# Optimization experiments

Measured on AMD Instinct MI355X. Metric: run time of the kernel, lower is better.

The kernel has to match this reference:

```python
import jax, jax.numpy as jnp
import numpy as np

G = 256          # voxel grid resolution per axis (single batch item)
N = 400000       # number of active voxels
C_IN, C_OUT = 32, 64
EPS = 1e-5


def _build_neighbor_maps():
    """Emulates torchsparse's hash-based kernel map for a 3x3x3, stride-1 conv.
    Returns int32 [27, N]: nbr_idx[k, i] = input voxel index at coords[i]+offset_k, or -1."""
    rng = np.random.default_rng(0)
    lin = rng.choice(G ** 3, size=N, replace=False).astype(np.int64)  # unique active voxels
    coords = np.stack(np.unravel_index(lin, (G, G, G)), axis=1)       # [N,3]
    order = np.argsort(lin)
    keys_sorted = lin[order]
    # 27 kernel offsets in {-1,0,1}^3
    offs = np.stack(np.meshgrid(*[np.arange(-1, 2)] * 3, indexing='ij'), axis=-1).reshape(27, 3)
    q = coords[None, :, :] + offs[:, None, :]                          # [27,N,3]
    inb = np.all((q >= 0) & (q < G), axis=-1)                          # [27,N]
    qc = np.clip(q, 0, G - 1)
    nk = (qc[..., 0] * G + qc[..., 1]) * G + qc[..., 2]                # [27,N]
    pos = np.searchsorted(keys_sorted, nk.ravel()).reshape(27, N)
    posc = np.minimum(pos, N - 1)
    found = inb & (keys_sorted[posc] == nk)
    nbr = np.where(found, order[posc], -1).astype(np.int32)
    return nbr


def setup_inputs() -> dict:
    key = jax.random.key(0)
    k1, k2 = jax.random.split(key)
    features = jax.random.normal(k1, (N, C_IN), dtype=jnp.float32)
    gamma = jnp.ones((C_IN,), jnp.float32)
    beta = jnp.zeros((C_IN,), jnp.float32)
    W = jax.random.normal(k2, (27, C_IN, C_OUT), dtype=jnp.float32) * 0.05
    nbr_idx = jnp.asarray(_build_neighbor_maps())
    return {"features": features, "gamma": gamma, "beta": beta, "W": W, "nbr_idx": nbr_idx}


def reference(features, gamma, beta, W, nbr_idx):
    # BatchNorm1d (training-mode batch stats) over active voxels
    mean = jnp.mean(features, axis=0)
    var = jnp.var(features, axis=0)
    x = gamma * (features - mean) * jax.lax.rsqrt(var + EPS) + beta
    x = jax.nn.relu(x)
    # Sparse 3x3x3 conv: per-offset gather -> GEMM -> accumulate (scatter is identity
    # since stride=1 keeps output coords == input coords).
    out0 = jnp.zeros((x.shape[0], W.shape[-1]), dtype=x.dtype)

    def body(acc, kw):
        idx, Wk = kw                                  # idx: [N], Wk: [C_in, C_out]
        valid = (idx >= 0)[:, None]
        g = jnp.where(valid, x[jnp.maximum(idx, 0)], 0.0)  # gather with masking
        return acc + g @ Wk, None

    out, _ = jax.lax.scan(body, out0, (nbr_idx, W))
    return out
```

## Files before the change

kernel.cpp:

```cpp
#include <hip/hip_runtime.h>
#include <hip/hip_bf16.h>

#define CIN  32
#define COUT 64
#define KVOL 27
#define FEPS 1e-5f

typedef __attribute__((ext_vector_type(8))) short short8;
typedef __attribute__((ext_vector_type(4))) float f32x4;


__device__ __forceinline__ unsigned bfr(float f) {
    unsigned u = __float_as_uint(f);
    return (u + 0x7FFFu + ((u >> 16) & 1u)) >> 16;
}

__global__ void k_zero(float* __restrict__ ws) {
    if (threadIdx.x < 64) ws[threadIdx.x] = 0.f;
}

__global__ __launch_bounds__(256) void k_reduce(const float* __restrict__ f,
                                                float* __restrict__ ws, int n4) {
    const float4* f4 = (const float4*)f;
    int tid    = blockIdx.x * blockDim.x + threadIdx.x;
    int stride = gridDim.x * blockDim.x;
    float4 s = make_float4(0.f, 0.f, 0.f, 0.f);
    float4 q = make_float4(0.f, 0.f, 0.f, 0.f);
    for (int i = tid; i < n4; i += stride) {
        float4 v = f4[i];
        s.x += v.x; s.y += v.y; s.z += v.z; s.w += v.w;
        q.x = fmaf(v.x, v.x, q.x); q.y = fmaf(v.y, v.y, q.y);
        q.z = fmaf(v.z, v.z, q.z); q.w = fmaf(v.w, v.w, q.w);
    }
    __shared__ float ls[64];
    if (threadIdx.x < 64) ls[threadIdx.x] = 0.f;
    __syncthreads();
    int g = threadIdx.x & 7;
    atomicAdd(&ls[g * 4 + 0], s.x); atomicAdd(&ls[g * 4 + 1], s.y);
    atomicAdd(&ls[g * 4 + 2], s.z); atomicAdd(&ls[g * 4 + 3], s.w);
    atomicAdd(&ls[32 + g * 4 + 0], q.x); atomicAdd(&ls[32 + g * 4 + 1], q.y);
    atomicAdd(&ls[32 + g * 4 + 2], q.z); atomicAdd(&ls[32 + g * 4 + 3], q.w);
    __syncthreads();
    if (threadIdx.x < 64) atomicAdd(&ws[threadIdx.x], ls[threadIdx.x]);
}

__global__ void k_final(const float* __restrict__ gamma, const float* __restrict__ beta,
                        float* __restrict__ ws, float invN) {
    int c = threadIdx.x;
    float mean = ws[c] * invN;
    float var  = fmaf(-mean, mean, ws[32 + c] * invN);
    float sc   = gamma[c] * rsqrtf(var + FEPS);
    ws[64 + c] = sc;
    ws[96 + c] = fmaf(-mean, sc, beta[c]);
}

__global__ __launch_bounds__(256) void k_norm(const float* __restrict__ f,
                                              const float* __restrict__ ws,
                                              uint4* __restrict__ xb, int n8) {
    const float4* f4 = (const float4*)f;
    int tid    = blockIdx.x * blockDim.x + threadIdx.x;
    int stride = gridDim.x * blockDim.x;
    int g = tid & 3;
    float4 s0 = ((const float4*)(ws + 64))[2 * g];
    float4 s1 = ((const float4*)(ws + 64))[2 * g + 1];
    float4 b0 = ((const float4*)(ws + 96))[2 * g];
    float4 b1 = ((const float4*)(ws + 96))[2 * g + 1];
    for (int i = tid; i < n8; i += stride) {
        float4 v0 = f4[2 * i], v1 = f4[2 * i + 1];
        v0.x = fmaxf(fmaf(v0.x, s0.x, b0.x), 0.f);
        v0.y = fmaxf(fmaf(v0.y, s0.y, b0.y), 0.f);
        v0.z = fmaxf(fmaf(v0.z, s0.z, b0.z), 0.f);
        v0.w = fmaxf(fmaf(v0.w, s0.w, b0.w), 0.f);
        v1.x = fmaxf(fmaf(v1.x, s1.x, b1.x), 0.f);
        v1.y = fmaxf(fmaf(v1.y, s1.y, b1.y), 0.f);
        v1.z = fmaxf(fmaf(v1.z, s1.z, b1.z), 0.f);
        v1.w = fmaxf(fmaf(v1.w, s1.w, b1.w), 0.f);
        uint4 r;
        r.x = bfr(v0.x) | (bfr(v0.y) << 16);
        r.y = bfr(v0.z) | (bfr(v0.w) << 16);
        r.z = bfr(v1.x) | (bfr(v1.y) << 16);
        r.w = bfr(v1.z) | (bfr(v1.w) << 16);
        xb[i] = r;
    }
}

__global__ __launch_bounds__(256) void k_prep(const float* __restrict__ W,
                                              uint4* __restrict__ Bf) {
    int k    = blockIdx.x;
    int nt   = threadIdx.x >> 6;
    int lane = threadIdx.x & 63;
    int col  = nt * 16 + (lane & 15);
    int kk   = (lane >> 4) * 8;
    const float* Wk = W + (size_t)k * (CIN * COUT);
    unsigned r[4];
#pragma unroll
    for (int e = 0; e < 4; ++e) {
        unsigned lo = bfr(Wk[(kk + 2 * e) * COUT + col]);
        unsigned hi = bfr(Wk[(kk + 2 * e + 1) * COUT + col]);
        r[e] = lo | (hi << 16);
    }
    Bf[(size_t)(k * 4 + nt) * 64 + lane] = make_uint4(r[0], r[1], r[2], r[3]);
}

#define GROUP_A(X) X(0,A) X(1,B) X(2,A) X(3,B) X(4,A) X(5,B) X(6,A) X(7,B) X(8,A)
#define GROUP_B(X) X(9,B) X(10,A) X(11,B) X(12,A) X(13,B) X(14,A) X(15,B) X(16,A) X(17,B)
#define GROUP_C(X) X(18,A) X(19,B) X(20,A) X(21,B) X(22,A) X(23,B) X(24,A) X(25,B) X(26,A)

#define KDECL(K,P) int idx##K; uint4 ga##K;
#define KIDX(K,P)  idx##K = nbrl[(size_t)(K) * n];
#define KGATH(K,P) ga##K = *(const uint4*)(xhb + ((size_t)((idx##K < 0) ? 0 : idx##K) << 6) + koff);
#define KPIN(K,P)  asm volatile("" : "+v"(ga##K.x), "+v"(ga##K.y), "+v"(ga##K.z), "+v"(ga##K.w));
#define KCONS(K,P) { uint4 z##K = (idx##K < 0) ? zero4 : ga##K;                                 \
    if (__ballot(idx##K >= 0)) {                                                                \
        short8 av = __builtin_bit_cast(short8, z##K);                                           \
        short8 b0 = __builtin_bit_cast(short8, Bs[(K) * 256 + lane]);                           \
        short8 b1 = __builtin_bit_cast(short8, Bs[(K) * 256 + 64 + lane]);                      \
        short8 b2 = __builtin_bit_cast(short8, Bs[(K) * 256 + 128 + lane]);                     \
        short8 b3 = __builtin_bit_cast(short8, Bs[(K) * 256 + 192 + lane]);                     \
        acc0##P = __builtin_amdgcn_mfma_f32_16x16x32_bf16(av, b0, acc0##P, 0, 0, 0);            \
        acc1##P = __builtin_amdgcn_mfma_f32_16x16x32_bf16(av, b1, acc1##P, 0, 0, 0);            \
        acc2##P = __builtin_amdgcn_mfma_f32_16x16x32_bf16(av, b2, acc2##P, 0, 0, 0);            \
        acc3##P = __builtin_amdgcn_mfma_f32_16x16x32_bf16(av, b3, acc3##P, 0, 0, 0);            \
    } }

__global__ __launch_bounds__(512, 2) void k_conv(const char* __restrict__ xhb,
                                                 const uint4* __restrict__ Bf,
                                                 const int* __restrict__ nbr,
                                                 float* __restrict__ out,
                                                 int n, int ntiles) {
    __shared__ uint4 Bs[KVOL * 256];
    int lane = threadIdx.x & 63;
    int wv   = threadIdx.x >> 6;

    for (int t = threadIdx.x; t < KVOL * 256; t += 512) Bs[t] = Bf[t];
    __syncthreads();

    int gw   = blockIdx.x * 8 + wv;
    int col  = lane & 15;
    int koff = (lane >> 4) * 16;
    const uint4 zero4 = make_uint4(0u, 0u, 0u, 0u);

    for (int t = gw; t < ntiles; t += 2048) {
        int r0 = t * 16;
        const int* nbrl = nbr + (r0 + col);

        f32x4 zf = {0.f, 0.f, 0.f, 0.f};
        f32x4 acc0A = zf, acc1A = zf, acc2A = zf, acc3A = zf;
        f32x4 acc0B = zf, acc1B = zf, acc2B = zf, acc3B = zf;

        GROUP_A(KDECL) GROUP_B(KDECL) GROUP_C(KDECL)
        GROUP_A(KIDX)  GROUP_B(KIDX)  GROUP_C(KIDX)
        GROUP_A(KGATH) GROUP_B(KGATH) GROUP_C(KGATH)
        GROUP_A(KPIN)
        GROUP_A(KCONS)
        GROUP_B(KPIN)
        GROUP_B(KCONS)
        GROUP_C(KPIN)
        GROUP_C(KCONS)

        f32x4 acc0 = acc0A + acc0B;
        f32x4 acc1 = acc1A + acc1B;
        f32x4 acc2 = acc2A + acc2B;
        f32x4 acc3 = acc3A + acc3B;

        int rbase = r0 + (lane >> 4) * 4;
        float* op = out + (size_t)rbase * COUT + col;
#pragma unroll
        for (int j = 0; j < 4; ++j) {
            op[j * COUT +  0] = acc0[j];
            op[j * COUT + 16] = acc1[j];
            op[j * COUT + 32] = acc2[j];
            op[j * COUT + 48] = acc3[j];
        }
    }
}

extern "C" void kernel_launch(void* const* d_in, const int* in_sizes, int n_in,
                              void* d_out, int out_size, void* d_ws, size_t ws_size,
                              hipStream_t stream) {
    const float* feat  = (const float*)d_in[0];
    const float* gamma = (const float*)d_in[1];
    const float* beta  = (const float*)d_in[2];
    const float* W     = (const float*)d_in[3];
    const int*   nbr   = (const int*)d_in[4];
    float* out = (float*)d_out;
    float* ws  = (float*)d_ws;

    int n  = in_sizes[0] / CIN;
    int n4 = in_sizes[0] / 4;
    int n8 = in_sizes[0] / 8;
    int ntiles = n / 16;
    uint4* Bf  = (uint4*)(ws + 128);
    uint4* xb  = (uint4*)(ws + 27776);
    char*  xhb = (char*)xb;

    hipLaunchKernelGGL(k_zero,   dim3(1), dim3(64), 0, stream, ws);
    hipLaunchKernelGGL(k_prep,   dim3(KVOL), dim3(256), 0, stream, W, Bf);
    hipLaunchKernelGGL(k_reduce, dim3(512), dim3(256), 0, stream, feat, ws, n4);
    hipLaunchKernelGGL(k_final,  dim3(1), dim3(32), 0, stream, gamma, beta, ws, 1.0f / (float)n);
    hipLaunchKernelGGL(k_norm,   dim3(2048), dim3(256), 0, stream, feat, ws, xb, n8);
    hipLaunchKernelGGL(k_conv,   dim3(256), dim3(512), 0, stream, xhb, Bf, nbr, out, n, ntiles);
}
```

Before: 94.40 us.

## Compact neighbor map into per-tile masks and packed pairs before conv

Adds a preprocessing kernel that turns the 27xN neighbor index table into a per-16-row-tile bitmask per offset plus a packed list of up to 64 (row, source index) pairs. The conv kernel then reads only these compact tile records and uses shuffles and popcounts to find each lane's source row. The centre offset is treated as the identity mapping, so its MFMA is done without any index lookup. The aim is to cut the per-lane index loads and their latency inside the conv loop. In exchange it adds a kernel launch and shuffle work. It also silently breaks if a tile has more than 64 valid neighbor pairs or if the centre offset is not the identity.

```diff
diff --git a/kernel.cpp b/kernel.cpp
--- a/kernel.cpp
+++ b/kernel.cpp
@@ -4,6 +4,7 @@
 #define CIN  32
 #define COUT 64
 #define KVOL 27
+#define KCEN 13
 #define FEPS 1e-5f
 
 typedef __attribute__((ext_vector_type(8))) short short8;
@@ -102,32 +103,71 @@
     Bf[(size_t)(k * 4 + nt) * 64 + lane] = make_uint4(r[0], r[1], r[2], r[3]);
 }
 
-#define GROUP_A(X) X(0,A) X(1,B) X(2,A) X(3,B) X(4,A) X(5,B) X(6,A) X(7,B) X(8,A)
-#define GROUP_B(X) X(9,B) X(10,A) X(11,B) X(12,A) X(13,B) X(14,A) X(15,B) X(16,A) X(17,B)
-#define GROUP_C(X) X(18,A) X(19,B) X(20,A) X(21,B) X(22,A) X(23,B) X(24,A) X(25,B) X(26,A)
-
-#define KDECL(K,P) int idx##K; uint4 ga##K;
-#define KIDX(K,P)  idx##K = nbrl[(size_t)(K) * n];
-#define KGATH(K,P) ga##K = *(const uint4*)(xhb + ((size_t)((idx##K < 0) ? 0 : idx##K) << 6) + koff);
+__global__ __launch_bounds__(256) void k_pre(const int* __restrict__ nbr,
+                                             unsigned* __restrict__ masks,
+                                             unsigned* __restrict__ pairs,
+                                             int n) {
+    int l  = threadIdx.x & 63;
+    int wv = threadIdx.x >> 6;
+    int v  = blockIdx.x * 256 + wv * 64 + l;
+    int q  = l >> 4;
+    int r  = l & 15;
+    int t  = v >> 4;
+    bool vok = (v < n);
+    int cnt = 0;
+#pragma unroll
+    for (int k = 0; k < KVOL; ++k) {
+        if (k == KCEN) {
+            if (vok && r == 0) masks[(size_t)t * 28 + k] = 0xFFFFu;
+            continue;
+        }
+        int idx = vok ? nbr[(size_t)k * n + v] : -1;
+        unsigned long long m64 = __ballot(idx >= 0);
+        unsigned m16 = (unsigned)(m64 >> (q * 16)) & 0xFFFFu;
+        if (vok && r == 0) masks[(size_t)t * 28 + k] = m16;
+        if (idx >= 0) {
+            int rank = __popc(m16 & ((1u << r) - 1u));
+            int pos  = cnt + rank;
+            if (pos < 64) pairs[(size_t)t * 64 + pos] = ((unsigned)r << 20) | (unsigned)idx;
+        }
+        cnt += __popc(m16);
+    }
+}
+
+#define SPARSE_A(X) X(0,A) X(1,B) X(2,A) X(3,B) X(4,A) X(5,B) X(6,A) X(7,B) X(8,A)
+#define SPARSE_B(X) X(9,B) X(10,A) X(11,B) X(12,A) X(14,B) X(15,A) X(16,B) X(17,A) X(18,B)
+#define SPARSE_C(X) X(19,A) X(20,B) X(21,A) X(22,B) X(23,A) X(24,B) X(25,A) X(26,B)
+
+#define KDECL(K,P) uint4 ga##K;
+#define KGATH(K,P) {                                                          \
+    unsigned mk = (unsigned)__shfl((int)maskv, (K));                          \
+    int j = prefix + __popc(mk & lanemask);                                   \
+    unsigned pw = (unsigned)__shfl((int)pairv, j & 63);                       \
+    int src = ((mk >> r) & 1u) ? (int)(pw & 0xFFFFFu) : 0;                    \
+    ga##K = *(const uint4*)(xhb + ((size_t)src << 6) + koff);                 \
+    prefix += __popc(mk); }
 #define KPIN(K,P)  asm volatile("" : "+v"(ga##K.x), "+v"(ga##K.y), "+v"(ga##K.z), "+v"(ga##K.w));
-#define KCONS(K,P) { uint4 z##K = (idx##K < 0) ? zero4 : ga##K;                                 \
-    if (__ballot(idx##K >= 0)) {                                                                \
-        short8 av = __builtin_bit_cast(short8, z##K);                                           \
-        short8 b0 = __builtin_bit_cast(short8, Bs[(K) * 256 + lane]);                           \
-        short8 b1 = __builtin_bit_cast(short8, Bs[(K) * 256 + 64 + lane]);                      \
-        short8 b2 = __builtin_bit_cast(short8, Bs[(K) * 256 + 128 + lane]);                     \
-        short8 b3 = __builtin_bit_cast(short8, Bs[(K) * 256 + 192 + lane]);                     \
-        acc0##P = __builtin_amdgcn_mfma_f32_16x16x32_bf16(av, b0, acc0##P, 0, 0, 0);            \
-        acc1##P = __builtin_amdgcn_mfma_f32_16x16x32_bf16(av, b1, acc1##P, 0, 0, 0);            \
-        acc2##P = __builtin_amdgcn_mfma_f32_16x16x32_bf16(av, b2, acc2##P, 0, 0, 0);            \
-        acc3##P = __builtin_amdgcn_mfma_f32_16x16x32_bf16(av, b3, acc3##P, 0, 0, 0);            \
+#define KCONS(K,P) {                                                          \
+    unsigned mk = (unsigned)__shfl((int)maskv, (K));                          \
+    if (__builtin_amdgcn_readfirstlane(mk)) {                                 \
+        uint4 z = ((mk >> r) & 1u) ? ga##K : zero4;                           \
+        short8 av = __builtin_bit_cast(short8, z);                            \
+        short8 b0 = __builtin_bit_cast(short8, Bs[(K) * 256 + lane]);         \
+        short8 b1 = __builtin_bit_cast(short8, Bs[(K) * 256 + 64 + lane]);    \
+        short8 b2 = __builtin_bit_cast(short8, Bs[(K) * 256 + 128 + lane]);   \
+        short8 b3 = __builtin_bit_cast(short8, Bs[(K) * 256 + 192 + lane]);   \
+        acc0##P = __builtin_amdgcn_mfma_f32_16x16x32_bf16(av, b0, acc0##P, 0, 0, 0); \
+        acc1##P = __builtin_amdgcn_mfma_f32_16x16x32_bf16(av, b1, acc1##P, 0, 0, 0); \
+        acc2##P = __builtin_amdgcn_mfma_f32_16x16x32_bf16(av, b2, acc2##P, 0, 0, 0); \
+        acc3##P = __builtin_amdgcn_mfma_f32_16x16x32_bf16(av, b3, acc3##P, 0, 0, 0); \
     } }
 
 __global__ __launch_bounds__(512, 2) void k_conv(const char* __restrict__ xhb,
                                                  const uint4* __restrict__ Bf,
-                                                 const int* __restrict__ nbr,
+                                                 const unsigned* __restrict__ masks,
+                                                 const unsigned* __restrict__ pairs,
                                                  float* __restrict__ out,
-                                                 int n, int ntiles) {
+                                                 int ntiles) {
     __shared__ uint4 Bs[KVOL * 256];
     int lane = threadIdx.x & 63;
     int wv   = threadIdx.x >> 6;
@@ -136,27 +176,45 @@
     __syncthreads();
 
     int gw   = blockIdx.x * 8 + wv;
-    int col  = lane & 15;
+    int r    = lane & 15;
+    unsigned lanemask = (1u << r) - 1u;
     int koff = (lane >> 4) * 16;
     const uint4 zero4 = make_uint4(0u, 0u, 0u, 0u);
 
     for (int t = gw; t < ntiles; t += 2048) {
         int r0 = t * 16;
-        const int* nbrl = nbr + (r0 + col);
+        int maskv = (lane < KVOL) ? (int)masks[(size_t)t * 28 + lane] : 0;
+        int pairv = (int)pairs[(size_t)t * 64 + lane];
+        int prefix = 0;
 
         f32x4 zf = {0.f, 0.f, 0.f, 0.f};
         f32x4 acc0A = zf, acc1A = zf, acc2A = zf, acc3A = zf;
         f32x4 acc0B = zf, acc1B = zf, acc2B = zf, acc3B = zf;
 
-        GROUP_A(KDECL) GROUP_B(KDECL) GROUP_C(KDECL)
-        GROUP_A(KIDX)  GROUP_B(KIDX)  GROUP_C(KIDX)
-        GROUP_A(KGATH) GROUP_B(KGATH) GROUP_C(KGATH)
-        GROUP_A(KPIN)
-        GROUP_A(KCONS)
-        GROUP_B(KPIN)
-        GROUP_B(KCONS)
-        GROUP_C(KPIN)
-        GROUP_C(KCONS)
+        SPARSE_A(KDECL) SPARSE_B(KDECL) SPARSE_C(KDECL)
+
+        uint4 ga13 = *(const uint4*)(xhb + ((size_t)(r0 + r) << 6) + koff);
+
+        SPARSE_A(KGATH) SPARSE_B(KGATH) SPARSE_C(KGATH)
+
+        {
+            short8 av = __builtin_bit_cast(short8, ga13);
+            short8 b0 = __builtin_bit_cast(short8, Bs[KCEN * 256 + lane]);
+            short8 b1 = __builtin_bit_cast(short8, Bs[KCEN * 256 + 64 + lane]);
+            short8 b2 = __builtin_bit_cast(short8, Bs[KCEN * 256 + 128 + lane]);
+            short8 b3 = __builtin_bit_cast(short8, Bs[KCEN * 256 + 192 + lane]);
+            acc0A = __builtin_amdgcn_mfma_f32_16x16x32_bf16(av, b0, acc0A, 0, 0, 0);
+            acc1A = __builtin_amdgcn_mfma_f32_16x16x32_bf16(av, b1, acc1A, 0, 0, 0);
+            acc2A = __builtin_amdgcn_mfma_f32_16x16x32_bf16(av, b2, acc2A, 0, 0, 0);
+            acc3A = __builtin_amdgcn_mfma_f32_16x16x32_bf16(av, b3, acc3A, 0, 0, 0);
+        }
+
+        SPARSE_A(KPIN)
+        SPARSE_A(KCONS)
+        SPARSE_B(KPIN)
+        SPARSE_B(KCONS)
+        SPARSE_C(KPIN)
+        SPARSE_C(KCONS)
 
         f32x4 acc0 = acc0A + acc0B;
         f32x4 acc1 = acc1A + acc1B;
@@ -164,7 +222,7 @@
         f32x4 acc3 = acc3A + acc3B;
 
         int rbase = r0 + (lane >> 4) * 4;
-        float* op = out + (size_t)rbase * COUT + col;
+        float* op = out + (size_t)rbase * COUT + r;
 #pragma unroll
         for (int j = 0; j < 4; ++j) {
             op[j * COUT +  0] = acc0[j];
@@ -193,11 +251,14 @@
     uint4* Bf  = (uint4*)(ws + 128);
     uint4* xb  = (uint4*)(ws + 27776);
     char*  xhb = (char*)xb;
+    unsigned* masks = (unsigned*)(ws + 27776 + (size_t)n * 16);
+    unsigned* pairs = masks + (size_t)ntiles * 28;
 
     hipLaunchKernelGGL(k_zero,   dim3(1), dim3(64), 0, stream, ws);
     hipLaunchKernelGGL(k_prep,   dim3(KVOL), dim3(256), 0, stream, W, Bf);
+    hipLaunchKernelGGL(k_pre,    dim3((n + 255) / 256), dim3(256), 0, stream, nbr, masks, pairs, n);
     hipLaunchKernelGGL(k_reduce, dim3(512), dim3(256), 0, stream, feat, ws, n4);
     hipLaunchKernelGGL(k_final,  dim3(1), dim3(32), 0, stream, gamma, beta, ws, 1.0f / (float)n);
     hipLaunchKernelGGL(k_norm,   dim3(2048), dim3(256), 0, stream, feat, ws, xb, n8);
-    hipLaunchKernelGGL(k_conv,   dim3(256), dim3(512), 0, stream, xhb, Bf, nbr, out, n, ntiles);
-}
+    hipLaunchKernelGGL(k_conv,   dim3(256), dim3(512), 0, stream, xhb, Bf, masks, pairs, out, ntiles);
+}
```

After: 123.6 us. 1.31x slower.

## Compact per-tile active kernel offsets and special-case the center offset

Applied to the files above, without the earlier changes.

A new pre-pass scans the neighbor map and, for each 16-row tile, writes a compacted list of encoded (offset, index) entries covering only offsets where some row in the tile has a valid neighbor, capped at 24. The conv kernel then handles the center offset directly as the identity gather, and loops over the compacted entries instead of all 27 offsets. It also swaps the MFMA operand order so the accumulators come out transposed, which allows float4 output stores. The aim is to cut wasted gathers and index loads for empty offsets. In exchange it adds an extra kernel and extra memory traffic for the entry table, assumes the center offset maps each voxel to itself, and silently drops offsets beyond the 24-entry cap.

```diff
diff --git a/kernel.cpp b/kernel.cpp
--- a/kernel.cpp
+++ b/kernel.cpp
@@ -4,7 +4,9 @@
 #define CIN  32
 #define COUT 64
 #define KVOL 27
+#define KCEN 13
 #define FEPS 1e-5f
+#define SENT 0xFFFFF
 
 typedef __attribute__((ext_vector_type(8))) short short8;
 typedef __attribute__((ext_vector_type(4))) float f32x4;
@@ -102,32 +104,74 @@
     Bf[(size_t)(k * 4 + nt) * 64 + lane] = make_uint4(r[0], r[1], r[2], r[3]);
 }
 
-#define GROUP_A(X) X(0,A) X(1,B) X(2,A) X(3,B) X(4,A) X(5,B) X(6,A) X(7,B) X(8,A)
-#define GROUP_B(X) X(9,B) X(10,A) X(11,B) X(12,A) X(13,B) X(14,A) X(15,B) X(16,A) X(17,B)
-#define GROUP_C(X) X(18,A) X(19,B) X(20,A) X(21,B) X(22,A) X(23,B) X(24,A) X(25,B) X(26,A)
-
-#define KDECL(K,P) int idx##K; uint4 ga##K;
-#define KIDX(K,P)  idx##K = nbrl[(size_t)(K) * n];
-#define KGATH(K,P) ga##K = *(const uint4*)(xhb + ((size_t)((idx##K < 0) ? 0 : idx##K) << 6) + koff);
-#define KPIN(K,P)  asm volatile("" : "+v"(ga##K.x), "+v"(ga##K.y), "+v"(ga##K.z), "+v"(ga##K.w));
-#define KCONS(K,P) { uint4 z##K = (idx##K < 0) ? zero4 : ga##K;                                 \
-    if (__ballot(idx##K >= 0)) {                                                                \
-        short8 av = __builtin_bit_cast(short8, z##K);                                           \
-        short8 b0 = __builtin_bit_cast(short8, Bs[(K) * 256 + lane]);                           \
-        short8 b1 = __builtin_bit_cast(short8, Bs[(K) * 256 + 64 + lane]);                      \
-        short8 b2 = __builtin_bit_cast(short8, Bs[(K) * 256 + 128 + lane]);                     \
-        short8 b3 = __builtin_bit_cast(short8, Bs[(K) * 256 + 192 + lane]);                     \
-        acc0##P = __builtin_amdgcn_mfma_f32_16x16x32_bf16(av, b0, acc0##P, 0, 0, 0);            \
-        acc1##P = __builtin_amdgcn_mfma_f32_16x16x32_bf16(av, b1, acc1##P, 0, 0, 0);            \
-        acc2##P = __builtin_amdgcn_mfma_f32_16x16x32_bf16(av, b2, acc2##P, 0, 0, 0);            \
-        acc3##P = __builtin_amdgcn_mfma_f32_16x16x32_bf16(av, b3, acc3##P, 0, 0, 0);            \
+__global__ __launch_bounds__(256) void k_cmp(const int* __restrict__ nbr,
+                                             int* __restrict__ ent,
+                                             int* __restrict__ cnt, int n) {
+    int l  = threadIdx.x & 63;
+    int wv = threadIdx.x >> 6;
+    int cb = (blockIdx.x * 4 + wv) * 256;
+    int v0 = cb + 4 * l;
+    bool vok = v0 < n;
+    int tl = l >> 2;
+    int T  = (cb >> 4) + tl;
+    int i4 = l & 3;
+    const int4* nbr4 = (const int4*)nbr;
+    int n4 = n >> 2;
+    int* eT = ent + (size_t)T * 384;
+    int c = 0;
+#pragma unroll
+    for (int k = 0; k < KVOL; ++k) {
+        if (k == KCEN) continue;
+        int4 v = vok ? nbr4[(size_t)k * n4 + (v0 >> 2)] : make_int4(-1, -1, -1, -1);
+        int e0 = (k << 20) | (v.x >= 0 ? v.x : SENT);
+        int e1 = (k << 20) | (v.y >= 0 ? v.y : SENT);
+        int e2 = (k << 20) | (v.z >= 0 ? v.z : SENT);
+        int e3 = (k << 20) | (v.w >= 0 ? v.w : SENT);
+        bool any = (v.x >= 0) || (v.y >= 0) || (v.z >= 0) || (v.w >= 0);
+        unsigned long long bal = __ballot(any);
+        bool anyT = ((bal >> (tl * 4)) & 0xFull) != 0;
+        if (anyT && c < 24) {
+            eT[(i4 * 4 + 0) * 24 + c] = e0;
+            eT[(i4 * 4 + 1) * 24 + c] = e1;
+            eT[(i4 * 4 + 2) * 24 + c] = e2;
+            eT[(i4 * 4 + 3) * 24 + c] = e3;
+        }
+        c += anyT ? 1 : 0;
+    }
+    if (vok && i4 == 0) cnt[T] = (c < 24) ? c : 24;
+}
+
+#define SLOTS(X) X(0, eA.x, A) X(1, eA.y, B) X(2, eA.z, A) X(3, eA.w, B)      \
+                 X(4, eB.x, A) X(5, eB.y, B) X(6, eB.z, A) X(7, eB.w, B)      \
+                 X(8, eC.x, A) X(9, eC.y, B) X(10, eC.z, A) X(11, eC.w, B)    \
+                 X(12, eD.x, A) X(13, eD.y, B) X(14, eD.z, A) X(15, eD.w, B)
+
+#define EGATH(J, EV, P) int ix##J = (EV) & SENT;                              \
+    ix##J = (ix##J < nvox) ? ix##J : 0;           \
+    uint4 ga##J = *(const uint4*)(xhb + ((size_t)ix##J << 6) + koff);
+#define EPIN(J, EV, P)  asm volatile("" : "+v"(ga##J.x), "+v"(ga##J.y), "+v"(ga##J.z), "+v"(ga##J.w));
+#define ECONS(J, EV, P) { bool cv##J = ((J) < cntv) && (((EV) & SENT) != SENT); \
+    if (__ballot(cv##J)) {                                                    \
+        uint4 z = cv##J ? ga##J : zero4;                                      \
+        short8 xv = __builtin_bit_cast(short8, z);                            \
+        int kk = ((EV) >> 20) & 31;                   \
+        const uint4* bp = &Bs[kk * 256 + lane];                               \
+        short8 w0 = __builtin_bit_cast(short8, bp[0]);                        \
+        short8 w1 = __builtin_bit_cast(short8, bp[64]);                       \
+        short8 w2 = __builtin_bit_cast(short8, bp[128]);                      \
+        short8 w3 = __builtin_bit_cast(short8, bp[192]);                      \
+        acc0##P = __builtin_amdgcn_mfma_f32_16x16x32_bf16(w0, xv, acc0##P, 0, 0, 0); \
+        acc1##P = __builtin_amdgcn_mfma_f32_16x16x32_bf16(w1, xv, acc1##P, 0, 0, 0); \
+        acc2##P = __builtin_amdgcn_mfma_f32_16x16x32_bf16(w2, xv, acc2##P, 0, 0, 0); \
+        acc3##P = __builtin_amdgcn_mfma_f32_16x16x32_bf16(w3, xv, acc3##P, 0, 0, 0); \
     } }
 
 __global__ __launch_bounds__(512, 2) void k_conv(const char* __restrict__ xhb,
                                                  const uint4* __restrict__ Bf,
-                                                 const int* __restrict__ nbr,
+                                                 const int* __restrict__ ent,
+                                                 const int* __restrict__ cnt,
                                                  float* __restrict__ out,
-                                                 int n, int ntiles) {
+                                                 int ntiles, int nvox) {
     __shared__ uint4 Bs[KVOL * 256];
     int lane = threadIdx.x & 63;
     int wv   = threadIdx.x >> 6;
@@ -136,42 +180,72 @@
     __syncthreads();
 
     int gw   = blockIdx.x * 8 + wv;
-    int col  = lane & 15;
+    int r    = lane & 15;
     int koff = (lane >> 4) * 16;
     const uint4 zero4 = make_uint4(0u, 0u, 0u, 0u);
 
     for (int t = gw; t < ntiles; t += 2048) {
         int r0 = t * 16;
-        const int* nbrl = nbr + (r0 + col);
+        const int* etp = ent + (size_t)t * 384 + r * 24;
+        const int4* et4 = (const int4*)etp;
+
+        int4 eA = et4[0], eB = et4[1], eC = et4[2], eD = et4[3];
+        int cntv = cnt[t];
+        uint4 gac = *(const uint4*)(xhb + ((size_t)(r0 + r) << 6) + koff);
 
         f32x4 zf = {0.f, 0.f, 0.f, 0.f};
         f32x4 acc0A = zf, acc1A = zf, acc2A = zf, acc3A = zf;
         f32x4 acc0B = zf, acc1B = zf, acc2B = zf, acc3B = zf;
 
-        GROUP_A(KDECL) GROUP_B(KDECL) GROUP_C(KDECL)
-        GROUP_A(KIDX)  GROUP_B(KIDX)  GROUP_C(KIDX)
-        GROUP_A(KGATH) GROUP_B(KGATH) GROUP_C(KGATH)
-        GROUP_A(KPIN)
-        GROUP_A(KCONS)
-        GROUP_B(KPIN)
-        GROUP_B(KCONS)
-        GROUP_C(KPIN)
-        GROUP_C(KCONS)
+        SLOTS(EGATH)
+        SLOTS(EPIN)
+
+        {
+            short8 xv = __builtin_bit_cast(short8, gac);
+            const uint4* bp = &Bs[KCEN * 256 + lane];
+            short8 w0 = __builtin_bit_cast(short8, bp[0]);
+            short8 w1 = __builtin_bit_cast(short8, bp[64]);
+            short8 w2 = __builtin_bit_cast(short8, bp[128]);
+            short8 w3 = __builtin_bit_cast(short8, bp[192]);
+            acc0A = __builtin_amdgcn_mfma_f32_16x16x32_bf16(w0, xv, acc0A, 0, 0, 0);
+            acc1A = __builtin_amdgcn_mfma_f32_16x16x32_bf16(w1, xv, acc1A, 0, 0, 0);
+            acc2A = __builtin_amdgcn_mfma_f32_16x16x32_bf16(w2, xv, acc2A, 0, 0, 0);
+            acc3A = __builtin_amdgcn_mfma_f32_16x16x32_bf16(w3, xv, acc3A, 0, 0, 0);
+        }
+
+        SLOTS(ECONS)
+
+        if (cntv > 16) {
+            for (int j = 16; j < cntv; ++j) {
+                int e = etp[j];
+                bool cv = ((e & SENT) != SENT);
+                int ix = e & SENT; ix = (ix < nvox) ? ix : 0;
+                uint4 z = cv ? *(const uint4*)(xhb + ((size_t)ix << 6) + koff) : zero4;
+                short8 xv = __builtin_bit_cast(short8, z);
+                int kk = (e >> 20) & 31;
+                const uint4* bp = &Bs[kk * 256 + lane];
+                short8 w0 = __builtin_bit_cast(short8, bp[0]);
+                short8 w1 = __builtin_bit_cast(short8, bp[64]);
+                short8 w2 = __builtin_bit_cast(short8, bp[128]);
+                short8 w3 = __builtin_bit_cast(short8, bp[192]);
+                acc0A = __builtin_amdgcn_mfma_f32_16x16x32_bf16(w0, xv, acc0A, 0, 0, 0);
+                acc1A = __builtin_amdgcn_mfma_f32_16x16x32_bf16(w1, xv, acc1A, 0, 0, 0);
+                acc2A = __builtin_amdgcn_mfma_f32_16x16x32_bf16(w2, xv, acc2A, 0, 0, 0);
+                acc3A = __builtin_amdgcn_mfma_f32_16x16x32_bf16(w3, xv, acc3A, 0, 0, 0);
+            }
+        }
 
         f32x4 acc0 = acc0A + acc0B;
         f32x4 acc1 = acc1A + acc1B;
         f32x4 acc2 = acc2A + acc2B;
         f32x4 acc3 = acc3A + acc3B;
 
-        int rbase = r0 + (lane >> 4) * 4;
-        float* op = out + (size_t)rbase * COUT + col;
-#pragma unroll
-        for (int j = 0; j < 4; ++j) {
-            op[j * COUT +  0] = acc0[j];
-            op[j * COUT + 16] = acc1[j];
-            op[j * COUT + 32] = acc2[j];
-            op[j * COUT + 48] = acc3[j];
-        }
+        int v = lane & 15, p = lane >> 4;
+        float4* ob = (float4*)(out + (size_t)(r0 + v) * COUT + p * 4);
+        ob[0]  = __builtin_bit_cast(float4, acc0);
+        ob[4]  = __builtin_bit_cast(float4, acc1);
+        ob[8]  = __builtin_bit_cast(float4, acc2);
+        ob[12] = __builtin_bit_cast(float4, acc3);
     }
 }
 
@@ -193,11 +267,14 @@
     uint4* Bf  = (uint4*)(ws + 128);
     uint4* xb  = (uint4*)(ws + 27776);
     char*  xhb = (char*)xb;
+    int*   ent = (int*)(ws + 27776 + (size_t)n * 16);
+    int*   cnt = ent + (size_t)ntiles * 384;
 
     hipLaunchKernelGGL(k_zero,   dim3(1), dim3(64), 0, stream, ws);
     hipLaunchKernelGGL(k_prep,   dim3(KVOL), dim3(256), 0, stream, W, Bf);
+    hipLaunchKernelGGL(k_cmp,    dim3((n + 1023) / 1024), dim3(256), 0, stream, nbr, ent, cnt, n);
     hipLaunchKernelGGL(k_reduce, dim3(512), dim3(256), 0, stream, feat, ws, n4);
     hipLaunchKernelGGL(k_final,  dim3(1), dim3(32), 0, stream, gamma, beta, ws, 1.0f / (float)n);
     hipLaunchKernelGGL(k_norm,   dim3(2048), dim3(256), 0, stream, feat, ws, xb, n8);
-    hipLaunchKernelGGL(k_conv,   dim3(256), dim3(512), 0, stream, xhb, Bf, nbr, out, n, ntiles);
-}
+    hipLaunchKernelGGL(k_conv,   dim3(256), dim3(512), 0, stream, xhb, Bf, ent, cnt, out, ntiles, n);
+}
```

New measurement: 148.2 us. +57.0%, slower.
